# Optimization experiments

Hardware: AMD Instinct MI355X
Metric: run time of the kernel (lower is better)

## Reference

```python
import jax, jax.numpy as jnp
import numpy as np

TEMPERATURE = 8.0  # sqrt(d_k) with d_k = 64


def setup_inputs() -> dict:
    key = jax.random.key(0)
    k1, k2, k3, k4 = jax.random.split(key, 4)
    B, S, D = 16, 2048, 64  # B = batch * n_heads
    q = jax.random.normal(k1, (B, S, D), dtype=jnp.float32)
    k = jax.random.normal(k2, (B, S, D), dtype=jnp.float32)
    v = jax.random.normal(k3, (B, S, D), dtype=jnp.float32)
    # boolean mask: True = masked out. Low prob so no row is fully masked.
    mask = jax.random.uniform(k4, (B, S, S)) < 0.1
    return {"q": q, "k": k, "v": v, "mask": mask}


def reference(q, k, v, mask):
    # attn = (q @ k^T) / temperature, masked_fill(mask, -inf), softmax over last dim
    attn = jnp.einsum("bqd,bkd->bqk", q, k) / TEMPERATURE
    attn = jnp.where(mask, -jnp.inf, attn)
    attn = jax.nn.softmax(attn, axis=2)
    output = jnp.einsum("bqk,bkd->bqd", attn, v)
    return output, attn
```

## Files before the change

kernel.cpp:

```cpp
#include <hip/hip_runtime.h>

typedef _Float16 half8 __attribute__((ext_vector_type(8)));
typedef _Float16 half4 __attribute__((ext_vector_type(4)));
typedef float    floatx4 __attribute__((ext_vector_type(4)));

#define NB  16
#define SEQ 2048
#define DIM 64
#define EST 2056

__global__ __launch_bounds__(256) void cvt_qk_kernel(const float* __restrict__ q,
                                                     const float* __restrict__ k,
                                                     _Float16* __restrict__ qh,
                                                     _Float16* __restrict__ kh) {
    size_t i = ((size_t)blockIdx.x * 256 + threadIdx.x) * 4;
    float4 a = *(const float4*)(q + i);
    float4 b = *(const float4*)(k + i);
    half4 ha = { (_Float16)a.x, (_Float16)a.y, (_Float16)a.z, (_Float16)a.w };
    half4 hb = { (_Float16)b.x, (_Float16)b.y, (_Float16)b.z, (_Float16)b.w };
    *(half4*)(qh + i) = ha;
    *(half4*)(kh + i) = hb;
}

__global__ __launch_bounds__(256) void cvt_vt_kernel(const float* __restrict__ v,
                                                     _Float16* __restrict__ vt) {
    __shared__ float tile[64][65];
    const int b  = blockIdx.x >> 5;
    const int s0 = (blockIdx.x & 31) << 6;
    const int t  = threadIdx.x;
    {
        const int row = t >> 2;
        const int c0  = (t & 3) << 4;
        const float* src = v + ((size_t)(b * SEQ + s0 + row)) * DIM + c0;
        #pragma unroll
        for (int i = 0; i < 4; ++i) {
            float4 x = *(const float4*)(src + i * 4);
            tile[row][c0 + i*4 + 0] = x.x;
            tile[row][c0 + i*4 + 1] = x.y;
            tile[row][c0 + i*4 + 2] = x.z;
            tile[row][c0 + i*4 + 3] = x.w;
        }
    }
    __syncthreads();
    {
        const int d  = t >> 2;
        const int sb = (t & 3) << 4;
        _Float16* dst = vt + ((size_t)(b * DIM + d)) * SEQ + s0 + sb;
        #pragma unroll
        for (int i = 0; i < 4; ++i) {
            half4 h = { (_Float16)tile[sb + i*4 + 0][d],
                        (_Float16)tile[sb + i*4 + 1][d],
                        (_Float16)tile[sb + i*4 + 2][d],
                        (_Float16)tile[sb + i*4 + 3][d] };
            *(half4*)(dst + i*4) = h;
        }
    }
}

__global__ __launch_bounds__(256) void attn_kernel(
    const _Float16* __restrict__ qh, const _Float16* __restrict__ kh,
    const _Float16* __restrict__ vt, const int* __restrict__ mask,
    float* __restrict__ out, float* __restrict__ attn)
{
    __shared__ _Float16 ebuf[16][EST];
    __shared__ float lsum[16];

    const int b    = blockIdx.x >> 7;
    const int r0   = (blockIdx.x & 127) << 4;
    const int lane = threadIdx.x & 63;
    const int wave = threadIdx.x >> 6;
    const int rl   = lane & 15;
    const int g    = lane >> 4;

    if (threadIdx.x < 16) lsum[threadIdx.x] = 0.0f;
    __syncthreads();

    const size_t qoff = ((size_t)(b * SEQ + r0 + rl)) * DIM + g * 8;
    half8 qa0 = *(const half8*)(qh + qoff);
    half8 qa1 = *(const half8*)(qh + qoff + 32);

    const _Float16* kbase = kh + (size_t)b * SEQ * DIM + (size_t)rl * DIM + g * 8;
    const int* mbase = mask + ((size_t)(b * SEQ + r0 + g * 4)) * SEQ + rl;

    float rs0 = 0.f, rs1 = 0.f, rs2 = 0.f, rs3 = 0.f;

    for (int jt = wave; jt < 128; jt += 4) {
        const int j0 = jt << 4;
        const _Float16* kp = kbase + (size_t)j0 * DIM;
        half8 kb0 = *(const half8*)kp;
        half8 kb1 = *(const half8*)(kp + 32);
        floatx4 c = {0.f, 0.f, 0.f, 0.f};
        c = __builtin_amdgcn_mfma_f32_16x16x32_f16(qa0, kb0, c, 0, 0, 0);
        c = __builtin_amdgcn_mfma_f32_16x16x32_f16(qa1, kb1, c, 0, 0, 0);
        const int* mp = mbase + j0;
        float e0 = mp[0]         ? 0.f : __expf(c[0] * 0.125f);
        float e1 = mp[SEQ]       ? 0.f : __expf(c[1] * 0.125f);
        float e2 = mp[2*SEQ]     ? 0.f : __expf(c[2] * 0.125f);
        float e3 = mp[3*SEQ]     ? 0.f : __expf(c[3] * 0.125f);
        rs0 += e0; rs1 += e1; rs2 += e2; rs3 += e3;
        ebuf[g*4 + 0][j0 + rl] = (_Float16)e0;
        ebuf[g*4 + 1][j0 + rl] = (_Float16)e1;
        ebuf[g*4 + 2][j0 + rl] = (_Float16)e2;
        ebuf[g*4 + 3][j0 + rl] = (_Float16)e3;
    }

    float rsv[4] = {rs0, rs1, rs2, rs3};
    #pragma unroll
    for (int i = 0; i < 4; ++i) {
        float v = rsv[i];
        v += __shfl_xor(v, 1);
        v += __shfl_xor(v, 2);
        v += __shfl_xor(v, 4);
        v += __shfl_xor(v, 8);
        if (rl == 0) atomicAdd(&lsum[g*4 + i], v);
    }
    __syncthreads();

    floatx4 oacc = {0.f, 0.f, 0.f, 0.f};
    const _Float16* vbase = vt + ((size_t)(b * DIM + wave * 16 + rl)) * SEQ + g * 8;
    #pragma unroll 4
    for (int jc = 0; jc < 64; ++jc) {
        half8 va = *(const half8*)(vbase + jc * 32);
        half8 eb = *(const half8*)(&ebuf[rl][jc * 32 + g * 8]);
        oacc = __builtin_amdgcn_mfma_f32_16x16x32_f16(va, eb, oacc, 0, 0, 0);
    }
    {
        const float inv = 1.0f / lsum[rl];
        floatx4 ov = { oacc[0]*inv, oacc[1]*inv, oacc[2]*inv, oacc[3]*inv };
        float* op = out + ((size_t)(b * SEQ + r0 + rl)) * DIM + wave * 16 + g * 4;
        *(floatx4*)op = ov;
    }

    {
        const int row  = threadIdx.x >> 4;
        const int cseg = threadIdx.x & 15;
        const float inv = 1.0f / lsum[row];
        float* ap = attn + ((size_t)(b * SEQ + r0 + row)) * SEQ;
        #pragma unroll
        for (int it = 0; it < 16; ++it) {
            const int c0 = cseg * 8 + it * 128;
            half8 ev = *(const half8*)(&ebuf[row][c0]);
            floatx4 lo = { (float)ev[0]*inv, (float)ev[1]*inv, (float)ev[2]*inv, (float)ev[3]*inv };
            floatx4 hi = { (float)ev[4]*inv, (float)ev[5]*inv, (float)ev[6]*inv, (float)ev[7]*inv };
            *(floatx4*)(ap + c0)     = lo;
            *(floatx4*)(ap + c0 + 4) = hi;
        }
    }
}

extern "C" void kernel_launch(void* const* d_in, const int* in_sizes, int n_in,
                              void* d_out, int out_size, void* d_ws, size_t ws_size,
                              hipStream_t stream) {
    const float* q = (const float*)d_in[0];
    const float* k = (const float*)d_in[1];
    const float* v = (const float*)d_in[2];
    const int* mask = (const int*)d_in[3];

    float* out  = (float*)d_out;
    float* attn = out + (size_t)NB * SEQ * DIM;

    _Float16* qh = (_Float16*)d_ws;
    _Float16* kh = qh + (size_t)NB * SEQ * DIM;
    _Float16* vt = kh + (size_t)NB * SEQ * DIM;

    cvt_qk_kernel<<<(NB * SEQ * DIM) / 1024, 256, 0, stream>>>(q, k, qh, kh);
    cvt_vt_kernel<<<NB * (SEQ / 64), 256, 0, stream>>>(v, vt);
    attn_kernel<<<NB * (SEQ / 16), 256, 0, stream>>>(qh, kh, vt, mask, out, attn);
}
```

Measured before the change: 617.8 us.

## Recompute QK^T in a second pass instead of buffering exp scores in LDS

Drops the 64KB per-block LDS buffer of exponentiated scores. The first pass now computes only row sums and packs the mask into bits held in registers. A second pass recomputes QK^T, writes normalised attention straight to global memory with nontemporal stores, and accumulates PV per wave over all 64 output columns, followed by a cross-wave reduction in LDS. The intent is higher occupancy (launch bounds of 4 blocks) and coalesced, vectorised mask loads, paid for with double the QK MFMA and exp work.

```diff
diff --git a/kernel.cpp b/kernel.cpp
--- a/kernel.cpp
+++ b/kernel.cpp
@@ -3,11 +3,13 @@
 typedef _Float16 half8 __attribute__((ext_vector_type(8)));
 typedef _Float16 half4 __attribute__((ext_vector_type(4)));
 typedef float    floatx4 __attribute__((ext_vector_type(4)));
+typedef int      intx4  __attribute__((ext_vector_type(4)));
 
 #define NB  16
 #define SEQ 2048
 #define DIM 64
-#define EST 2056
+
+#define MFMA(a,b,c) __builtin_amdgcn_mfma_f32_16x16x32_f16((a),(b),(c),0,0,0)
 
 __global__ __launch_bounds__(256) void cvt_qk_kernel(const float* __restrict__ q,
                                                      const float* __restrict__ k,
@@ -57,13 +59,14 @@
     }
 }
 
-__global__ __launch_bounds__(256) void attn_kernel(
+__global__ __launch_bounds__(256, 4) void attn_kernel(
     const _Float16* __restrict__ qh, const _Float16* __restrict__ kh,
     const _Float16* __restrict__ vt, const int* __restrict__ mask,
     float* __restrict__ out, float* __restrict__ attn)
 {
-    __shared__ _Float16 ebuf[16][EST];
-    __shared__ float lsum[16];
+    __shared__ float wsum[4][16];
+    __shared__ __align__(16) _Float16 tsc[4][16][40];
+    __shared__ __align__(16) float outred[4][16][68];
 
     const int b    = blockIdx.x >> 7;
     const int r0   = (blockIdx.x & 127) << 4;
@@ -72,79 +75,132 @@
     const int rl   = lane & 15;
     const int g    = lane >> 4;
 
-    if (threadIdx.x < 16) lsum[threadIdx.x] = 0.0f;
+    const size_t qoff = ((size_t)(b * SEQ + r0 + rl)) * DIM + g * 8;
+    const half8 qa0 = *(const half8*)(qh + qoff);
+    const half8 qa1 = *(const half8*)(qh + qoff + 32);
+
+    const _Float16* kbase = kh + (size_t)b * SEQ * DIM + (size_t)rl * DIM + g * 8;
+    const int*      mbase = mask + ((size_t)(b * SEQ + r0 + rl)) * SEQ + g * 4;
+
+    float rs = 0.f;
+    uint32_t mb0 = 0, mb1 = 0, mb2 = 0, mb3 = 0;
+
+    intx4 pm0 = __builtin_nontemporal_load((const intx4*)(mbase + wave * 32));
+    intx4 pm1 = __builtin_nontemporal_load((const intx4*)(mbase + wave * 32 + 16));
+
+    for (int cc = 0; cc < 16; ++cc) {
+        const int jj = (cc * 4 + wave) * 32;
+        const intx4 m0 = pm0, m1 = pm1;
+        if (cc < 15) {
+            pm0 = __builtin_nontemporal_load((const intx4*)(mbase + jj + 128));
+            pm1 = __builtin_nontemporal_load((const intx4*)(mbase + jj + 128 + 16));
+        }
+        const _Float16* kp = kbase + (size_t)jj * DIM;
+        half8 ka0 = *(const half8*)(kp);
+        half8 ka1 = *(const half8*)(kp + 32);
+        half8 kb0 = *(const half8*)(kp + 16 * DIM);
+        half8 kb1 = *(const half8*)(kp + 16 * DIM + 32);
+        floatx4 c0 = {0.f,0.f,0.f,0.f}, c1 = {0.f,0.f,0.f,0.f};
+        c0 = MFMA(ka0, qa0, c0);
+        c0 = MFMA(ka1, qa1, c0);
+        c1 = MFMA(kb0, qa0, c1);
+        c1 = MFMA(kb1, qa1, c1);
+        float e0 = m0.x ? 0.f : __expf(c0[0] * 0.125f);
+        float e1 = m0.y ? 0.f : __expf(c0[1] * 0.125f);
+        float e2 = m0.z ? 0.f : __expf(c0[2] * 0.125f);
+        float e3 = m0.w ? 0.f : __expf(c0[3] * 0.125f);
+        float e4 = m1.x ? 0.f : __expf(c1[0] * 0.125f);
+        float e5 = m1.y ? 0.f : __expf(c1[1] * 0.125f);
+        float e6 = m1.z ? 0.f : __expf(c1[2] * 0.125f);
+        float e7 = m1.w ? 0.f : __expf(c1[3] * 0.125f);
+        rs += (e0 + e1) + (e2 + e3) + (e4 + e5) + (e6 + e7);
+        uint32_t byt = (m0.x ? 1u : 0u)        | ((m0.y ? 1u : 0u) << 1)
+                     | ((m0.z ? 1u : 0u) << 2) | ((m0.w ? 1u : 0u) << 3)
+                     | ((m1.x ? 1u : 0u) << 4) | ((m1.y ? 1u : 0u) << 5)
+                     | ((m1.z ? 1u : 0u) << 6) | ((m1.w ? 1u : 0u) << 7);
+        mb0 = (mb0 >> 8) | (mb1 << 24);
+        mb1 = (mb1 >> 8) | (mb2 << 24);
+        mb2 = (mb2 >> 8) | (mb3 << 24);
+        mb3 = (mb3 >> 8) | (byt << 24);
+    }
+
+    rs += __shfl_xor(rs, 16);
+    rs += __shfl_xor(rs, 32);
+    if (g == 0) wsum[wave][rl] = rs;
     __syncthreads();
-
-    const size_t qoff = ((size_t)(b * SEQ + r0 + rl)) * DIM + g * 8;
-    half8 qa0 = *(const half8*)(qh + qoff);
-    half8 qa1 = *(const half8*)(qh + qoff + 32);
-
-    const _Float16* kbase = kh + (size_t)b * SEQ * DIM + (size_t)rl * DIM + g * 8;
-    const int* mbase = mask + ((size_t)(b * SEQ + r0 + g * 4)) * SEQ + rl;
-
-    float rs0 = 0.f, rs1 = 0.f, rs2 = 0.f, rs3 = 0.f;
-
-    for (int jt = wave; jt < 128; jt += 4) {
-        const int j0 = jt << 4;
-        const _Float16* kp = kbase + (size_t)j0 * DIM;
-        half8 kb0 = *(const half8*)kp;
-        half8 kb1 = *(const half8*)(kp + 32);
-        floatx4 c = {0.f, 0.f, 0.f, 0.f};
-        c = __builtin_amdgcn_mfma_f32_16x16x32_f16(qa0, kb0, c, 0, 0, 0);
-        c = __builtin_amdgcn_mfma_f32_16x16x32_f16(qa1, kb1, c, 0, 0, 0);
-        const int* mp = mbase + j0;
-        float e0 = mp[0]         ? 0.f : __expf(c[0] * 0.125f);
-        float e1 = mp[SEQ]       ? 0.f : __expf(c[1] * 0.125f);
-        float e2 = mp[2*SEQ]     ? 0.f : __expf(c[2] * 0.125f);
-        float e3 = mp[3*SEQ]     ? 0.f : __expf(c[3] * 0.125f);
-        rs0 += e0; rs1 += e1; rs2 += e2; rs3 += e3;
-        ebuf[g*4 + 0][j0 + rl] = (_Float16)e0;
-        ebuf[g*4 + 1][j0 + rl] = (_Float16)e1;
-        ebuf[g*4 + 2][j0 + rl] = (_Float16)e2;
-        ebuf[g*4 + 3][j0 + rl] = (_Float16)e3;
-    }
-
-    float rsv[4] = {rs0, rs1, rs2, rs3};
-    #pragma unroll
-    for (int i = 0; i < 4; ++i) {
-        float v = rsv[i];
-        v += __shfl_xor(v, 1);
-        v += __shfl_xor(v, 2);
-        v += __shfl_xor(v, 4);
-        v += __shfl_xor(v, 8);
-        if (rl == 0) atomicAdd(&lsum[g*4 + i], v);
-    }
+    const float inv = 1.0f / (wsum[0][rl] + wsum[1][rl] + wsum[2][rl] + wsum[3][rl]);
+
+    floatx4 o0 = {0.f,0.f,0.f,0.f}, o1 = {0.f,0.f,0.f,0.f};
+    floatx4 o2 = {0.f,0.f,0.f,0.f}, o3 = {0.f,0.f,0.f,0.f};
+    const _Float16* vbase = vt + ((size_t)b * DIM + rl) * SEQ + g * 8;
+    float* abase = attn + ((size_t)(b * SEQ + r0 + rl)) * SEQ + g * 4;
+
+    for (int cc = 0; cc < 16; ++cc) {
+        const int jj = (cc * 4 + wave) * 32;
+        const _Float16* kp = kbase + (size_t)jj * DIM;
+        half8 ka0 = *(const half8*)(kp);
+        half8 ka1 = *(const half8*)(kp + 32);
+        half8 kb0 = *(const half8*)(kp + 16 * DIM);
+        half8 kb1 = *(const half8*)(kp + 16 * DIM + 32);
+        floatx4 c0 = {0.f,0.f,0.f,0.f}, c1 = {0.f,0.f,0.f,0.f};
+        c0 = MFMA(ka0, qa0, c0);
+        c0 = MFMA(ka1, qa1, c0);
+        c1 = MFMA(kb0, qa0, c1);
+        c1 = MFMA(kb1, qa1, c1);
+
+        const uint32_t byt = mb0 & 0xffu;
+        mb0 = (mb0 >> 8) | (mb1 << 24);
+        mb1 = (mb1 >> 8) | (mb2 << 24);
+        mb2 = (mb2 >> 8) | (mb3 << 24);
+        mb3 =  mb3 >> 8;
+
+        float e0 = (byt & 1u)   ? 0.f : __expf(c0[0] * 0.125f);
+        float e1 = (byt & 2u)   ? 0.f : __expf(c0[1] * 0.125f);
+        float e2 = (byt & 4u)   ? 0.f : __expf(c0[2] * 0.125f);
+        float e3 = (byt & 8u)   ? 0.f : __expf(c0[3] * 0.125f);
+        float e4 = (byt & 16u)  ? 0.f : __expf(c1[0] * 0.125f);
+        float e5 = (byt & 32u)  ? 0.f : __expf(c1[1] * 0.125f);
+        float e6 = (byt & 64u)  ? 0.f : __expf(c1[2] * 0.125f);
+        float e7 = (byt & 128u) ? 0.f : __expf(c1[3] * 0.125f);
+
+        floatx4 a0 = { e0 * inv, e1 * inv, e2 * inv, e3 * inv };
+        floatx4 a1 = { e4 * inv, e5 * inv, e6 * inv, e7 * inv };
+        __builtin_nontemporal_store(a0, (floatx4*)(abase + jj));
+        __builtin_nontemporal_store(a1, (floatx4*)(abase + jj + 16));
+
+        half4 h0 = { (_Float16)e0, (_Float16)e1, (_Float16)e2, (_Float16)e3 };
+        half4 h1 = { (_Float16)e4, (_Float16)e5, (_Float16)e6, (_Float16)e7 };
+        *(half4*)(&tsc[wave][rl][g * 4])      = h0;
+        *(half4*)(&tsc[wave][rl][16 + g * 4]) = h1;
+        half8 eb = *(const half8*)(&tsc[wave][rl][g * 8]);
+
+        const _Float16* vp = vbase + jj;
+        half8 v0 = *(const half8*)(vp);
+        half8 v1 = *(const half8*)(vp + 16 * SEQ);
+        half8 v2 = *(const half8*)(vp + 32 * SEQ);
+        half8 v3 = *(const half8*)(vp + 48 * SEQ);
+        o0 = MFMA(v0, eb, o0);
+        o1 = MFMA(v1, eb, o1);
+        o2 = MFMA(v2, eb, o2);
+        o3 = MFMA(v3, eb, o3);
+    }
+
+    *(floatx4*)(&outred[wave][rl][ 0 + g * 4]) = o0;
+    *(floatx4*)(&outred[wave][rl][16 + g * 4]) = o1;
+    *(floatx4*)(&outred[wave][rl][32 + g * 4]) = o2;
+    *(floatx4*)(&outred[wave][rl][48 + g * 4]) = o3;
     __syncthreads();
-
-    floatx4 oacc = {0.f, 0.f, 0.f, 0.f};
-    const _Float16* vbase = vt + ((size_t)(b * DIM + wave * 16 + rl)) * SEQ + g * 8;
-    #pragma unroll 4
-    for (int jc = 0; jc < 64; ++jc) {
-        half8 va = *(const half8*)(vbase + jc * 32);
-        half8 eb = *(const half8*)(&ebuf[rl][jc * 32 + g * 8]);
-        oacc = __builtin_amdgcn_mfma_f32_16x16x32_f16(va, eb, oacc, 0, 0, 0);
-    }
     {
-        const float inv = 1.0f / lsum[rl];
-        floatx4 ov = { oacc[0]*inv, oacc[1]*inv, oacc[2]*inv, oacc[3]*inv };
-        float* op = out + ((size_t)(b * SEQ + r0 + rl)) * DIM + wave * 16 + g * 4;
-        *(floatx4*)op = ov;
-    }
-
-    {
-        const int row  = threadIdx.x >> 4;
-        const int cseg = threadIdx.x & 15;
-        const float inv = 1.0f / lsum[row];
-        float* ap = attn + ((size_t)(b * SEQ + r0 + row)) * SEQ;
-        #pragma unroll
-        for (int it = 0; it < 16; ++it) {
-            const int c0 = cseg * 8 + it * 128;
-            half8 ev = *(const half8*)(&ebuf[row][c0]);
-            floatx4 lo = { (float)ev[0]*inv, (float)ev[1]*inv, (float)ev[2]*inv, (float)ev[3]*inv };
-            floatx4 hi = { (float)ev[4]*inv, (float)ev[5]*inv, (float)ev[6]*inv, (float)ev[7]*inv };
-            *(floatx4*)(ap + c0)     = lo;
-            *(floatx4*)(ap + c0 + 4) = hi;
-        }
+        const int r  = threadIdx.x >> 4;
+        const int c4 = (threadIdx.x & 15) << 2;
+        floatx4 s0 = *(const floatx4*)(&outred[0][r][c4]);
+        floatx4 s1 = *(const floatx4*)(&outred[1][r][c4]);
+        floatx4 s2 = *(const floatx4*)(&outred[2][r][c4]);
+        floatx4 s3 = *(const floatx4*)(&outred[3][r][c4]);
+        floatx4 s = (s0 + s1) + (s2 + s3);
+        const float inv2 = 1.0f / (wsum[0][r] + wsum[1][r] + wsum[2][r] + wsum[3][r]);
+        floatx4 ov = { s[0] * inv2, s[1] * inv2, s[2] * inv2, s[3] * inv2 };
+        *(floatx4*)(out + ((size_t)(b * SEQ + r0 + r)) * DIM + c4) = ov;
     }
 }
 
```

After: 652.9 us. 1.06x slower.
